# Optimization experiments

Hardware: AMD Instinct MI355X
Metric: run time of the kernel (lower is better)

## Reference

```python
import jax, jax.numpy as jnp
import numpy as np

PAD_ID, SOS_ID, EOS_ID = 0, 1, 2


def setup_inputs() -> dict:
    key = jax.random.key(0)
    ks = jax.random.split(key, 8)
    V, E, H, B = 16000, 256, 512, 8
    s = 0.05  # weight scale to keep softmax well-conditioned
    return {
        "hidden": jax.random.normal(ks[0], (1, B, H), dtype=jnp.float32),
        "embedding": jax.random.normal(ks[1], (V, E), dtype=jnp.float32) * s,
        "w_ih": jax.random.normal(ks[2], (3 * H, E), dtype=jnp.float32) * s,
        "w_hh": jax.random.normal(ks[3], (3 * H, H), dtype=jnp.float32) * s,
        "b_ih": jax.random.normal(ks[4], (3 * H,), dtype=jnp.float32) * s,
        "b_hh": jax.random.normal(ks[5], (3 * H,), dtype=jnp.float32) * s,
        "w_out": jax.random.normal(ks[6], (V, H), dtype=jnp.float32) * s,
        "b_out": jax.random.normal(ks[7], (V,), dtype=jnp.float32) * s,
        "lenseq": 12,
        "k": 5,
    }


def reference(hidden, embedding, w_ih, w_hh, b_ih, b_hh, w_out, b_out, lenseq, k):
    V, E = embedding.shape
    _, B, H = hidden.shape
    dt = hidden.dtype
    pad_onehot = jax.nn.one_hot(PAD_ID, V, dtype=dt)

    def gru_cell(x_emb, h):  # x_emb: (k,B,E), h: (k,B,H); torch nn.GRU gate order r,z,n
        gi = x_emb @ w_ih.T + b_ih
        gh = h @ w_hh.T + b_hh
        i_r, i_z, i_n = jnp.split(gi, 3, axis=-1)
        h_r, h_z, h_n = jnp.split(gh, 3, axis=-1)
        r = jax.nn.sigmoid(i_r + h_r)
        z = jax.nn.sigmoid(i_z + h_z)
        n = jnp.tanh(i_n + r * h_n)
        return (1.0 - z) * n + z * h

    def step(carry, i):
        x, h, prob, res, _ = carry
        done = (x == EOS_ID) | (x == PAD_ID)            # (k,B)
        emb = embedding[x]                               # (k,B,E)
        h_new = gru_cell(emb, h)                         # (k,B,H)
        probs = jax.nn.softmax(h_new @ w_out.T + b_out, axis=-1)  # (k,B,V)
        pred = jnp.where(done[..., None], pad_onehot, probs)
        h = jnp.where(done[..., None], h, h_new)
        res = res.at[:, i].set(pred)                     # store raw pred (pre prob-scaling), as torch.cat copies
        scores = pred * prob[..., None]                  # (k,B,V); prob stays all-ones, faithful to source
        flat = scores.transpose(1, 0, 2).reshape(B, k * V)  # beam-major flatten per batch elem
        _, idx = jax.lax.top_k(flat, k)                  # (B,k)
        beam = (idx // V).T                              # (k,B)
        tok = (idx % V).T                                # (k,B)
        res = jnp.take_along_axis(res, beam[:, None, :, None], axis=0)
        prob = jnp.take_along_axis(prob, beam, axis=0)
        h = jnp.take_along_axis(h, beam[..., None], axis=0)
        return (tok, h, prob, res, pred), None

    x0 = jnp.full((k, B), SOS_ID, dtype=jnp.int32)
    h0 = jnp.broadcast_to(hidden[0], (k, B, H))
    prob0 = jnp.ones((k, B), dtype=dt)
    res0 = jnp.zeros((k, lenseq, B, V), dtype=dt)
    pred0 = jnp.zeros((k, B, V), dtype=dt)

    (x, h, prob, res, pred), _ = jax.lax.scan(step, (x0, h0, prob0, res0, pred0), jnp.arange(lenseq))

    # final top-1 selection per batch element over (k*V) flat scores
    scores = pred * prob[..., None]
    flat = scores.transpose(1, 0, 2).reshape(B, k * V)
    best_beam = jnp.argmax(flat, axis=-1) // V           # (B,)
    out = jnp.take_along_axis(res, best_beam[None, None, :, None], axis=0)[0]  # (lenseq,B,V)
    return out
```

## Files before the change

kernel.cpp:

```cpp
#include <hip/hip_runtime.h>

#define V 16000
#define E 256
#define H 512
#define HP 516
#define BB 8
#define T 12
#define NB 250
#define NBS 256
#define TPB 1024
#define CPB 64
#define BBH (BB * H)
#define AGENT __HIP_MEMORY_SCOPE_AGENT

typedef float vfloat4 __attribute__((ext_vector_type(4)));


constexpr int W_FL   = CPB * 512;
constexpr int SH_OFF = W_FL;
constexpr int SP_OFF = SH_OFF + BB * HP;
constexpr int RS_OFF = SP_OFF + 64 * 48;
constexpr int RV_OFF = RS_OFF + 128;
constexpr int RI_OFF = RV_OFF + 128;
constexpr int SS_OFF = RI_OFF + 128;
constexpr int XN_OFF = SS_OFF + 8;
constexpr int X_OFF  = XN_OFF + 8;
constexpr int SMEM_FL = X_OFF + 8;
constexpr size_t SMEM_BYTES = (size_t)SMEM_FL * 4;

__device__ __forceinline__ float dot4(float4 a, float4 b) {
    return a.x * b.x + a.y * b.y + a.z * b.z + a.w * b.w;
}

__global__ __launch_bounds__(256) void kinit(const float* __restrict__ hidden,
                                             float* __restrict__ hbuf,
                                             int* __restrict__ leaf,
                                             int* __restrict__ epoch) {
    int idx = blockIdx.x * 256 + threadIdx.x;
    if (idx < BBH) hbuf[idx] = hidden[idx];
    if (idx < 64 * 16) leaf[idx] = 0;
    if (idx == 0) epoch[0] = 0;
}

__device__ __forceinline__ void gridbar(int* __restrict__ leaf,
                                        int* __restrict__ epoch, int ep) {
    __syncthreads();
    if (threadIdx.x == 0) {
        int g = blockIdx.x >> 2;
        __hip_atomic_fetch_add(&leaf[g * 16], 1, __ATOMIC_RELEASE, AGENT);
    }
    if (blockIdx.x == 0) {
        if (threadIdx.x < 63) {
            int expct = (threadIdx.x == 62) ? 2 : 4;
            while (__hip_atomic_load(&leaf[threadIdx.x * 16],
                                     __ATOMIC_RELAXED, AGENT) < expct * ep)
                __builtin_amdgcn_s_sleep(1);
        }
        __syncthreads();
        if (threadIdx.x == 0)
            __hip_atomic_store(epoch, ep, __ATOMIC_RELAXED, AGENT);
    } else {
        if (threadIdx.x == 0) {
            while (__hip_atomic_load(epoch, __ATOMIC_RELAXED, AGENT) < ep)
                __builtin_amdgcn_s_sleep(1);
        }
    }
    __builtin_amdgcn_fence(__ATOMIC_ACQUIRE, "workgroup");
    __syncthreads();
}

__global__ __launch_bounds__(TPB, 4) void kmain(
    const float* __restrict__ emb_tab,
    const float* __restrict__ w_ih,
    const float* __restrict__ w_hh,
    const float* __restrict__ b_ih,
    const float* __restrict__ b_hh,
    const float* __restrict__ w_out,
    const float* __restrict__ b_out,
    float* __restrict__ hbuf,
    float* __restrict__ pq,
    int* __restrict__ leaf,
    int* __restrict__ epoch,
    float* __restrict__ out)
{
    extern __shared__ float smem[];
    float* w_lds  = smem;
    float* s_h    = smem + SH_OFF;
    float* s_part = smem + SP_OFF;
    float* s_e    = smem + SP_OFF;
    float* s_rsum = smem + RS_OFF;
    float* s_rval = smem + RV_OFF;
    int*   s_ridx = (int*)(smem + RI_OFF);
    float* s_S    = smem + SS_OFF;
    int*   s_Xn   = (int*)(smem + XN_OFF);
    int*   s_X    = (int*)(smem + X_OFF);

    const int blk = blockIdx.x, tid = threadIdx.x;

    for (int i = tid; i < CPB * 128; i += TPB) {
        int col = i >> 7;
        int q4  = (i & 127) << 2;
        int vv  = blk * CPB + col;
        float4 w4 = *(const float4*)(w_out + (size_t)vv * H + q4);
        int sw = q4 ^ ((col & 7) << 2) ^ (((q4 >> 5) & 7) << 2);
        *(float4*)(w_lds + col * 512 + sw) = w4;
    }
    if (tid < BB) s_X[tid] = 1;
    __syncthreads();

    const int lane = tid & 63;
    const int wv   = tid >> 6;
    const int rh   = lane & 3;
    const int kq   = (lane >> 2) & 15;
    const int rowhalf = wv & 1;
    const int cs   = wv >> 1;
    const int r    = rowhalf * 4 + rh;
    const int xw   = (cs ^ (kq & 7)) << 2;
    const int hswz = (kq & 7) << 2;

    float bo[8];
#pragma unroll
    for (int p = 0; p < 8; p++) bo[p] = b_out[blk * CPB + p * 8 + cs];

    for (int t = 0; t < T; t++) {
        const float* h_cur = hbuf + (size_t)t * BBH;
        float*       h_nxt = hbuf + (size_t)(t + 1) * BBH;

        if (blk < 64) {
            int hr = tid >> 7, k4 = (tid & 127) << 2;
            *(float4*)(s_h + hr * HP + k4) =
                *(const float4*)(h_cur + hr * H + k4);
        }
        __syncthreads();
        if (blk < 64 && tid < 512) {
            const int jl = tid >> 6;
            const int ar = (tid >> 3) & 7;
            const int kq8 = tid & 7;
            const int j  = blk * 8 + jl;
            const int pair = jl * 8 + ar;
            float gir = 0.f, giz = 0.f, gin = 0.f, ghr = 0.f, ghz = 0.f, ghn = 0.f;
            {
                const float* erow = emb_tab + (size_t)s_X[ar] * E;
                const float* w0 = w_ih + (size_t)j * E;
                const float* w1 = w0 + (size_t)H * E;
                const float* w2 = w1 + (size_t)H * E;
                const int k0 = kq8 * (E / 8);
                for (int k = 0; k < E / 8; k += 4) {
                    float4 ev = *(const float4*)(erow + k0 + k);
                    gir += dot4(*(const float4*)(w0 + k0 + k), ev);
                    giz += dot4(*(const float4*)(w1 + k0 + k), ev);
                    gin += dot4(*(const float4*)(w2 + k0 + k), ev);
                }
            }
            {
                const float* hrow = s_h + ar * HP;
                const float* w0 = w_hh + (size_t)j * H;
                const float* w1 = w0 + (size_t)H * H;
                const float* w2 = w1 + (size_t)H * H;
                const int k0 = kq8 * (H / 8);
                for (int k = 0; k < H / 8; k += 4) {
                    float4 hv = *(const float4*)(hrow + k0 + k);
                    ghr += dot4(*(const float4*)(w0 + k0 + k), hv);
                    ghz += dot4(*(const float4*)(w1 + k0 + k), hv);
                    ghn += dot4(*(const float4*)(w2 + k0 + k), hv);
                }
            }
            float* sp = s_part + pair * 48;
            sp[0 * 8 + kq8] = gir; sp[1 * 8 + kq8] = giz; sp[2 * 8 + kq8] = gin;
            sp[3 * 8 + kq8] = ghr; sp[4 * 8 + kq8] = ghz; sp[5 * 8 + kq8] = ghn;
        }
        __syncthreads();
        if (blk < 64 && tid < 512 && (tid & 7) == 0) {
            const int pair = (tid >> 6) * 8 + ((tid >> 3) & 7);
            const int jl = pair >> 3, ar = pair & 7;
            const int j  = blk * 8 + jl;
            const float* sp2 = s_part + pair * 48;
            float G[6];
#pragma unroll
            for (int gg = 0; gg < 6; gg++) {
                float s = 0.f;
#pragma unroll
                for (int q = 0; q < 8; q++) s += sp2[gg * 8 + q];
                G[gg] = s;
            }
            float ir  = G[0] + b_ih[j],         hr_ = G[3] + b_hh[j];
            float iz  = G[1] + b_ih[H + j],     hz  = G[4] + b_hh[H + j];
            float inn = G[2] + b_ih[2 * H + j], hn  = G[5] + b_hh[2 * H + j];
            float rg = 1.f / (1.f + __expf(-(ir + hr_)));
            float zg = 1.f / (1.f + __expf(-(iz + hz)));
            float ng = tanhf(inn + rg * hn);
            float ho = s_h[ar * HP + j];
            int xr = s_X[ar];
            bool dn = (xr == 0) || (xr == 2);
            float hv = dn ? ho : ((1.f - zg) * ng + zg * ho);
            h_nxt[ar * H + j] = hv;
        }
        gridbar(leaf, epoch, 2 * t + 1);

        {
            int hr = tid >> 7, k4 = (tid & 127) << 2;
            float4 hv4 = *(const float4*)(h_nxt + hr * H + k4);
            int sw = k4 ^ (((k4 >> 5) & 7) << 2);
            *(float4*)(s_h + hr * HP + sw) = hv4;
        }
        __syncthreads();
        {
            float4 hreg[8];
            const float* hb = s_h + r * HP + kq * 32;
#pragma unroll
            for (int i = 0; i < 8; i++)
                hreg[i] = *(const float4*)(hb + ((4 * i) ^ hswz));

            float s_acc = 0.f, bv = -1.f; int bi = 0x7fffffff;
#pragma unroll
            for (int p = 0; p < 8; p++) {
                const int col = p * 8 + cs;
                const int vv  = blk * CPB + col;
                const float* wb = w_lds + col * 512 + kq * 32;
                float acc = 0.f;
#pragma unroll
                for (int i = 0; i < 8; i++) {
                    float4 w4 = *(const float4*)(wb + ((4 * i) ^ xw));
                    acc += dot4(w4, hreg[i]);
                }
                acc += __shfl_xor(acc, 4, 64);
                acc += __shfl_xor(acc, 8, 64);
                acc += __shfl_xor(acc, 16, 64);
                acc += __shfl_xor(acc, 32, 64);
                float ee = __expf(acc + bo[p]);
                if (kq == 0) s_e[r * 65 + col] = ee;
                s_acc += ee;
                if (ee > bv) { bv = ee; bi = vv; }
            }
            if (kq == 0) {
                s_rsum[wv * 8 + r] = s_acc;
                s_rval[wv * 8 + r] = bv;
                s_ridx[wv * 8 + r] = bi;
            } else if (kq == 1) {
                int ro = (1 - rowhalf) * 4 + rh;
                s_rsum[wv * 8 + ro] = 0.f;
                s_rval[wv * 8 + ro] = -1.f;
                s_ridx[wv * 8 + ro] = 0x7fffffff;
            }
        }
        __syncthreads();
        if (tid < 64) {
            float s  = s_rsum[tid] + s_rsum[tid + 64];
            float av = s_rval[tid], bv2 = s_rval[tid + 64];
            int   ai = s_ridx[tid], bi2 = s_ridx[tid + 64];
            float bv = av; int bi = ai;
            if (bv2 > bv || (bv2 == bv && bi2 < bi)) { bv = bv2; bi = bi2; }
#pragma unroll
            for (int m = 8; m <= 32; m <<= 1) {
                s += __shfl_xor(s, m, 64);
                float ov = __shfl_xor(bv, m, 64);
                int   oi = __shfl_xor(bi, m, 64);
                if (ov > bv || (ov == bv && oi < bi)) { bv = ov; bi = oi; }
            }
            if (tid < 8) {
                vfloat4 q;
                q.x = s; q.y = bv; q.z = __int_as_float(bi); q.w = 0.f;
                *(vfloat4*)(pq + ((size_t)(t * 8 + tid) * NBS + blk) * 4) = q;
            }
        }
        gridbar(leaf, epoch, 2 * t + 2);

        if (wv < 8) {
            const float* pqt = pq + (size_t)(t * 8 + wv) * NBS * 4;
            float s = 0.f, bv = -1.f; int bi = 0x7fffffff;
#pragma unroll
            for (int c = 0; c < 4; c++) {
                int idx = lane + 64 * c;
                if (idx < NB) {
                    vfloat4 q = *(const vfloat4*)(pqt + (size_t)idx * 4);
                    s += q.x;
                    float ov = q.y;
                    int   oi = __float_as_int(q.z);
                    if (ov > bv || (ov == bv && oi < bi)) { bv = ov; bi = oi; }
                }
            }
            for (int m = 1; m < 64; m <<= 1) {
                s += __shfl_xor(s, m, 64);
                float ov = __shfl_xor(bv, m, 64);
                int   oi = __shfl_xor(bi, m, 64);
                if (ov > bv || (ov == bv && oi < bi)) { bv = ov; bi = oi; }
            }
            if (lane == 0) { s_S[wv] = s; s_Xn[wv] = bi; }
        }
        __syncthreads();
        {
            float* out_t = out + (size_t)t * BB * V;
            if (tid < 128) {
                int row = tid >> 4;
                int c4  = (tid & 15) << 2;
                int xr = s_X[row];
                bool dn = (xr == 0) || (xr == 2);
                float inv = 1.f / s_S[row];
                int vbase = blk * CPB + c4;
                vfloat4 o4;
                o4.x = dn ? ((vbase + 0 == 0) ? 1.f : 0.f) : s_e[row * 65 + c4 + 0] * inv;
                o4.y = dn ? ((vbase + 1 == 0) ? 1.f : 0.f) : s_e[row * 65 + c4 + 1] * inv;
                o4.z = dn ? ((vbase + 2 == 0) ? 1.f : 0.f) : s_e[row * 65 + c4 + 2] * inv;
                o4.w = dn ? ((vbase + 3 == 0) ? 1.f : 0.f) : s_e[row * 65 + c4 + 3] * inv;
                __builtin_nontemporal_store(o4,
                    (vfloat4*)(out_t + (size_t)row * V + vbase));
            }
        }
        __syncthreads();
        if (tid < 8) {
            int xo = s_X[tid];
            s_X[tid] = ((xo == 0) || (xo == 2)) ? 0 : s_Xn[tid];
        }
        __syncthreads();
    }
}

extern "C" void kernel_launch(void* const* d_in, const int* in_sizes, int n_in,
                              void* d_out, int out_size, void* d_ws, size_t ws_size,
                              hipStream_t stream) {
    (void)in_sizes; (void)n_in; (void)out_size; (void)ws_size;
    const float* hidden    = (const float*)d_in[0];
    const float* embedding = (const float*)d_in[1];
    const float* w_ih      = (const float*)d_in[2];
    const float* w_hh      = (const float*)d_in[3];
    const float* b_ih      = (const float*)d_in[4];
    const float* b_hh      = (const float*)d_in[5];
    const float* w_out     = (const float*)d_in[6];
    const float* b_out     = (const float*)d_in[7];
    float* out = (float*)d_out;

    float* ws    = (float*)d_ws;
    float* hbuf  = ws;
    float* pq    = hbuf + (size_t)(T + 1) * BBH;
    int*   leaf  = (int*)(pq + (size_t)T * 8 * NBS * 4);
    int*   epoch = leaf + 64 * 16;

    hipFuncSetAttribute((const void*)kmain,
        hipFuncAttributeMaxDynamicSharedMemorySize,
        (int)SMEM_BYTES);

    kinit<<<16, 256, 0, stream>>>(hidden, hbuf, leaf, epoch);
    kmain<<<NB, TPB, SMEM_BYTES, stream>>>(embedding, w_ih, w_hh, b_ih, b_hh,
                                           w_out, b_out, hbuf, pq,
                                           leaf, epoch, out);
}
```

Baseline: 612.2 us.

## Split grid barrier so only GRU-producing blocks arrive; use atomic cross-block transfers

Replaces the single grid barrier after the GRU stage with a barrier where only the 64 blocks that write the new hidden state arrive, so the root waits on 16 counters instead of 63. The hidden state and partial top-k results are now written and read with relaxed agent-scope atomic 64-bit loads and stores, with the GRU outputs first staged in LDS and then packed. The aim is to shorten barrier latency per step. The cost is extra LDS staging, an additional syncthreads, and split atomic loads in place of vector loads.

```diff
diff --git a/kernel.cpp b/kernel.cpp
--- a/kernel.cpp
+++ b/kernel.cpp
@@ -14,6 +14,7 @@
 #define AGENT __HIP_MEMORY_SCOPE_AGENT
 
 typedef float vfloat4 __attribute__((ext_vector_type(4)));
+typedef unsigned long long u64;
 
 
 constexpr int W_FL   = CPB * 512;
@@ -28,40 +29,63 @@
 constexpr int SMEM_FL = X_OFF + 8;
 constexpr size_t SMEM_BYTES = (size_t)SMEM_FL * 4;
 
+constexpr int CNT_LINES = 84;
+
 __device__ __forceinline__ float dot4(float4 a, float4 b) {
     return a.x * b.x + a.y * b.y + a.z * b.z + a.w * b.w;
 }
 
 __global__ __launch_bounds__(256) void kinit(const float* __restrict__ hidden,
                                              float* __restrict__ hbuf,
-                                             int* __restrict__ leaf,
-                                             int* __restrict__ epoch) {
+                                             int* __restrict__ cnt) {
     int idx = blockIdx.x * 256 + threadIdx.x;
     if (idx < BBH) hbuf[idx] = hidden[idx];
-    if (idx < 64 * 16) leaf[idx] = 0;
-    if (idx == 0) epoch[0] = 0;
-}
-
-__device__ __forceinline__ void gridbar(int* __restrict__ leaf,
-                                        int* __restrict__ epoch, int ep) {
+    if (idx < CNT_LINES * 16) cnt[idx] = 0;
+}
+
+__device__ __forceinline__ void barA(int* __restrict__ cnt, int ep) {
+    __syncthreads();
+    if (blockIdx.x < 64 && threadIdx.x == 0)
+        __hip_atomic_fetch_add(&cnt[(64 + (blockIdx.x >> 2)) * 16], 1,
+                               __ATOMIC_RELEASE, AGENT);
+    if (blockIdx.x == 0) {
+        if (threadIdx.x < 16) {
+            while (__hip_atomic_load(&cnt[(64 + threadIdx.x) * 16],
+                                     __ATOMIC_RELAXED, AGENT) < 4 * ep)
+                __builtin_amdgcn_s_sleep(1);
+        }
+        __syncthreads();
+        if (threadIdx.x == 0)
+            __hip_atomic_store(&cnt[63 * 16], ep, __ATOMIC_RELAXED, AGENT);
+    } else {
+        if (threadIdx.x == 0) {
+            while (__hip_atomic_load(&cnt[63 * 16], __ATOMIC_RELAXED, AGENT) < ep)
+                __builtin_amdgcn_s_sleep(1);
+        }
+    }
+    __builtin_amdgcn_fence(__ATOMIC_ACQUIRE, "workgroup");
+    __syncthreads();
+}
+
+__device__ __forceinline__ void barB(int* __restrict__ cnt, int ep) {
     __syncthreads();
     if (threadIdx.x == 0) {
         int g = blockIdx.x >> 2;
-        __hip_atomic_fetch_add(&leaf[g * 16], 1, __ATOMIC_RELEASE, AGENT);
+        __hip_atomic_fetch_add(&cnt[g * 16], 1, __ATOMIC_RELEASE, AGENT);
     }
     if (blockIdx.x == 0) {
         if (threadIdx.x < 63) {
             int expct = (threadIdx.x == 62) ? 2 : 4;
-            while (__hip_atomic_load(&leaf[threadIdx.x * 16],
+            while (__hip_atomic_load(&cnt[threadIdx.x * 16],
                                      __ATOMIC_RELAXED, AGENT) < expct * ep)
                 __builtin_amdgcn_s_sleep(1);
         }
         __syncthreads();
         if (threadIdx.x == 0)
-            __hip_atomic_store(epoch, ep, __ATOMIC_RELAXED, AGENT);
+            __hip_atomic_store(&cnt[80 * 16], ep, __ATOMIC_RELAXED, AGENT);
     } else {
         if (threadIdx.x == 0) {
-            while (__hip_atomic_load(epoch, __ATOMIC_RELAXED, AGENT) < ep)
+            while (__hip_atomic_load(&cnt[80 * 16], __ATOMIC_RELAXED, AGENT) < ep)
                 __builtin_amdgcn_s_sleep(1);
         }
     }
@@ -78,9 +102,9 @@
     const float* __restrict__ w_out,
     const float* __restrict__ b_out,
     float* __restrict__ hbuf,
-    float* __restrict__ pq,
-    int* __restrict__ leaf,
-    int* __restrict__ epoch,
+    u64* __restrict__ pqm,
+    int* __restrict__ pqi,
+    int* __restrict__ cnt,
     float* __restrict__ out)
 {
     extern __shared__ float smem[];
@@ -128,8 +152,12 @@
 
         if (blk < 64) {
             int hr = tid >> 7, k4 = (tid & 127) << 2;
+            const u64* p = (const u64*)(h_cur + hr * H + k4);
+            union { u64 u; float f[2]; } c0, c1;
+            c0.u = __hip_atomic_load(p,     __ATOMIC_RELAXED, AGENT);
+            c1.u = __hip_atomic_load(p + 1, __ATOMIC_RELAXED, AGENT);
             *(float4*)(s_h + hr * HP + k4) =
-                *(const float4*)(h_cur + hr * H + k4);
+                make_float4(c0.f[0], c0.f[1], c1.f[0], c1.f[1]);
         }
         __syncthreads();
         if (blk < 64 && tid < 512) {
@@ -193,15 +221,28 @@
             int xr = s_X[ar];
             bool dn = (xr == 0) || (xr == 2);
             float hv = dn ? ho : ((1.f - zg) * ng + zg * ho);
-            h_nxt[ar * H + j] = hv;
-        }
-        gridbar(leaf, epoch, 2 * t + 1);
+            s_rsum[ar * 8 + jl] = hv;
+        }
+        __syncthreads();
+        if (blk < 64 && tid < 32) {
+            int ar = tid >> 2, q2 = (tid & 3) << 1;
+            union { float f[2]; u64 u; } pk;
+            pk.f[0] = s_rsum[ar * 8 + q2];
+            pk.f[1] = s_rsum[ar * 8 + q2 + 1];
+            __hip_atomic_store((u64*)(h_nxt + (size_t)ar * H + blk * 8 + q2),
+                               pk.u, __ATOMIC_RELAXED, AGENT);
+        }
+        barA(cnt, t + 1);
 
         {
             int hr = tid >> 7, k4 = (tid & 127) << 2;
-            float4 hv4 = *(const float4*)(h_nxt + hr * H + k4);
+            const u64* p = (const u64*)(h_nxt + hr * H + k4);
+            union { u64 u; float f[2]; } c0, c1;
+            c0.u = __hip_atomic_load(p,     __ATOMIC_RELAXED, AGENT);
+            c1.u = __hip_atomic_load(p + 1, __ATOMIC_RELAXED, AGENT);
             int sw = k4 ^ (((k4 >> 5) & 7) << 2);
-            *(float4*)(s_h + hr * HP + sw) = hv4;
+            *(float4*)(s_h + hr * HP + sw) =
+                make_float4(c0.f[0], c0.f[1], c1.f[0], c1.f[1]);
         }
         __syncthreads();
         {
@@ -258,24 +299,29 @@
                 if (ov > bv || (ov == bv && oi < bi)) { bv = ov; bi = oi; }
             }
             if (tid < 8) {
-                vfloat4 q;
-                q.x = s; q.y = bv; q.z = __int_as_float(bi); q.w = 0.f;
-                *(vfloat4*)(pq + ((size_t)(t * 8 + tid) * NBS + blk) * 4) = q;
-            }
-        }
-        gridbar(leaf, epoch, 2 * t + 2);
+                union { float f[2]; u64 u; } pk;
+                pk.f[0] = s; pk.f[1] = bv;
+                size_t o = (size_t)(t * 8 + tid) * NBS + blk;
+                __hip_atomic_store(&pqm[o], pk.u, __ATOMIC_RELAXED, AGENT);
+                __hip_atomic_store(&pqi[o], bi,   __ATOMIC_RELAXED, AGENT);
+            }
+        }
+        barB(cnt, t + 1);
 
         if (wv < 8) {
-            const float* pqt = pq + (size_t)(t * 8 + wv) * NBS * 4;
+            const size_t base = (size_t)(t * 8 + wv) * NBS;
             float s = 0.f, bv = -1.f; int bi = 0x7fffffff;
 #pragma unroll
             for (int c = 0; c < 4; c++) {
                 int idx = lane + 64 * c;
                 if (idx < NB) {
-                    vfloat4 q = *(const vfloat4*)(pqt + (size_t)idx * 4);
-                    s += q.x;
-                    float ov = q.y;
-                    int   oi = __float_as_int(q.z);
+                    union { float f[2]; u64 u; } pk;
+                    pk.u = __hip_atomic_load(&pqm[base + idx],
+                                             __ATOMIC_RELAXED, AGENT);
+                    s += pk.f[0];
+                    float ov = pk.f[1];
+                    int   oi = __hip_atomic_load(&pqi[base + idx],
+                                                 __ATOMIC_RELAXED, AGENT);
                     if (ov > bv || (ov == bv && oi < bi)) { bv = ov; bi = oi; }
                 }
             }
@@ -331,16 +377,16 @@
 
     float* ws    = (float*)d_ws;
     float* hbuf  = ws;
-    float* pq    = hbuf + (size_t)(T + 1) * BBH;
-    int*   leaf  = (int*)(pq + (size_t)T * 8 * NBS * 4);
-    int*   epoch = leaf + 64 * 16;
+    u64*   pqm   = (u64*)(hbuf + (size_t)(T + 1) * BBH);
+    int*   pqi   = (int*)(pqm + (size_t)T * 8 * NBS);
+    int*   cnt   = pqi + (size_t)T * 8 * NBS;
 
     hipFuncSetAttribute((const void*)kmain,
         hipFuncAttributeMaxDynamicSharedMemorySize,
         (int)SMEM_BYTES);
 
-    kinit<<<16, 256, 0, stream>>>(hidden, hbuf, leaf, epoch);
+    kinit<<<16, 256, 0, stream>>>(hidden, hbuf, cnt);
     kmain<<<NB, TPB, SMEM_BYTES, stream>>>(embedding, w_ih, w_hh, b_ih, b_hh,
-                                           w_out, b_out, hbuf, pq,
-                                           leaf, epoch, out);
-}
+                                           w_out, b_out, hbuf, pqm, pqi,
+                                           cnt, out);
+}
```

Result: faster. 558.6 us (-8.7%).
